# Performance work log

Measured on AMD Instinct MI355X. Metric: run time of the kernel, lower is better.

The kernel has to match this reference:

```python
import jax, jax.numpy as jnp
import numpy as np

N_E, E_DIM, BETA = 1024, 64, 0.25

def setup_inputs() -> dict:
    key = jax.random.key(0)
    k1, k2 = jax.random.split(key)
    z = jax.random.normal(k1, (16, 4096, E_DIM), dtype=jnp.float32)
    embedding = jax.random.uniform(k2, (N_E, E_DIM), dtype=jnp.float32,
                                   minval=-1.0 / 256, maxval=1.0 / 256)
    return {"z": z, "embedding": embedding}

def reference(z, embedding):
    # z: [B, S, D]; embedding: [n_e, D]
    zf = z.reshape(-1, E_DIM)  # [N, D]
    # squared euclidean distances: ||z||^2 + ||e||^2 - 2 z e^T -> [N, n_e]
    d = (jnp.sum(zf * zf, axis=1, keepdims=True)
         + jnp.sum(embedding * embedding, axis=1)
         - 2.0 * jnp.matmul(zf, embedding.T))
    min_encoding_indices = jnp.argmin(d, axis=1)  # [N]
    z_q = embedding[min_encoding_indices].reshape(z.shape)  # [B, S, D]
    sg = jax.lax.stop_gradient
    loss = (jnp.mean((z_q - sg(z)) ** 2)
            + BETA * jnp.mean((sg(z_q) - z) ** 2))
    z_q = z + sg(z_q - z)  # straight-through estimator
    return (loss, z_q, min_encoding_indices)
```

## Files before the change

### kernel.cpp

```cpp
#include <hip/hip_runtime.h>


#define D 64
#define NE 1024
#define SEGS 8
#define CPS 128
#define ROWS 64
#define TPB 512
#define LDS_STRIDE 68

__global__ __launch_bounds__(TPB, 6) void vq_kernel(const float* __restrict__ z,
                                                    const float* __restrict__ emb,
                                                    float* __restrict__ out_loss,
                                                    float* __restrict__ out_zq,
                                                    float* __restrict__ out_idx,
                                                    float loss_scale) {
    __shared__ float lds_z[ROWS * LDS_STRIDE];
    __shared__ float ee_lds[NE];
    __shared__ float smv[SEGS * ROWS];
    __shared__ int   smi[SEGS * ROWS];

    const int tid = threadIdx.x;
    const size_t blockRow = (size_t)blockIdx.x * ROWS;

    const float4* zg4 = (const float4*)(z + blockRow * D);
#pragma unroll
    for (int it = 0; it < 2; ++it) {
        int i = it * TPB + tid;
        int row = i >> 4, col = i & 15;
        float4 v = zg4[i];
        *(float4*)&lds_z[row * LDS_STRIDE + col * 4] = v;
    }

    {
#pragma clang fp contract(off)
#pragma unroll
        for (int cc = 0; cc < 2; ++cc) {
            const int j = tid + cc * TPB;
            const float4* e4 = (const float4*)(emb + ((size_t)j << 6));
            float4 a = e4[0], b = e4[1];
            float r[8];
            r[0] = a.x*a.x; r[1] = a.y*a.y; r[2] = a.z*a.z; r[3] = a.w*a.w;
            r[4] = b.x*b.x; r[5] = b.y*b.y; r[6] = b.z*b.z; r[7] = b.w*b.w;
#pragma unroll
            for (int g = 1; g < 8; ++g) {
                float4 c = e4[2*g], e = e4[2*g + 1];
                r[0] = r[0] + c.x*c.x; r[1] = r[1] + c.y*c.y;
                r[2] = r[2] + c.z*c.z; r[3] = r[3] + c.w*c.w;
                r[4] = r[4] + e.x*e.x; r[5] = r[5] + e.y*e.y;
                r[6] = r[6] + e.z*e.z; r[7] = r[7] + e.w*e.w;
            }
            ee_lds[j] = ((r[0]+r[1]) + (r[2]+r[3])) + ((r[4]+r[5]) + (r[6]+r[7]));
        }
    }
    __syncthreads();

    const int rrow = tid & (ROWS - 1);
    const int seg  = tid >> 6;

    float zr[D];
#pragma unroll
    for (int c = 0; c < 16; ++c) {
        float4 v = *(const float4*)&lds_z[rrow * LDS_STRIDE + c * 4];
        zr[4*c+0] = v.x; zr[4*c+1] = v.y; zr[4*c+2] = v.z; zr[4*c+3] = v.w;
    }

    float zz;
    {
#pragma clang fp contract(off)
        float r[8];
#pragma unroll
        for (int jj = 0; jj < 8; ++jj) { float t = zr[jj] * zr[jj]; r[jj] = t; }
#pragma unroll
        for (int i = 8; i < 64; i += 8) {
#pragma unroll
            for (int jj = 0; jj < 8; ++jj) { float t = zr[i+jj] * zr[i+jj]; r[jj] = r[jj] + t; }
        }
        zz = ((r[0]+r[1]) + (r[2]+r[3])) + ((r[4]+r[5]) + (r[6]+r[7]));
    }

    float minv = __builtin_inff();
    int mini = 0;
    const int jbase = __builtin_amdgcn_readfirstlane(seg * CPS);
#pragma unroll 2
    for (int jj = 0; jj < CPS; ++jj) {
        const int j = jbase + jj;
        const float4* ew4 = (const float4*)(emb + ((size_t)j << 6));
        float p0 = 0.f, p1 = 0.f, p2 = 0.f, p3 = 0.f;
#pragma unroll
        for (int c = 0; c < 16; ++c) {
            float4 e4 = ew4[c];
            p0 = fmaf(zr[4*c+0], e4.x, p0);
            p1 = fmaf(zr[4*c+1], e4.y, p1);
            p2 = fmaf(zr[4*c+2], e4.z, p2);
            p3 = fmaf(zr[4*c+3], e4.w, p3);
        }
        float dot = (p0 + p1) + (p2 + p3);
        float t1 = zz + ee_lds[j];
        float d = fmaf(-2.0f, dot, t1);
        if (d < minv) { minv = d; mini = j; }
    }

    smv[seg * ROWS + rrow] = minv;
    smi[seg * ROWS + rrow] = mini;
    __syncthreads();

    if (tid < ROWS) {
        float best = __builtin_inff();
        int bi = 0;
#pragma unroll
        for (int s = 0; s < SEGS; ++s) {
            float v = smv[s * ROWS + rrow];
            if (v < best) { best = v; bi = smi[s * ROWS + rrow]; }
        }

        const float4* qe4 = (const float4*)(emb + ((size_t)bi << 6));
        float s = 0.f;
#pragma unroll
        for (int c = 0; c < 16; ++c) {
            float4 q = qe4[c];
            float z0 = zr[4*c+0], z1 = zr[4*c+1], z2 = zr[4*c+2], z3 = zr[4*c+3];
            float d0 = q.x - z0, d1 = q.y - z1, d2 = q.z - z2, d3 = q.w - z3;
            s += d0*d0; s += d1*d1; s += d2*d2; s += d3*d3;
            float4 o;
            o.x = z0 + d0; o.y = z1 + d1; o.z = z2 + d2; o.w = z3 + d3;
            *(float4*)&lds_z[rrow * LDS_STRIDE + c * 4] = o;
        }
        out_idx[blockRow + rrow] = (float)bi;

#pragma unroll
        for (int off = 32; off; off >>= 1) s += __shfl_down(s, off);
        if (tid == 0) atomicAdd(out_loss, s * loss_scale);
    }
    __syncthreads();

    const size_t obase = blockRow * D;
#pragma unroll
    for (int it = 0; it < 8; ++it) {
        int i = it * TPB + tid;
        int row = i >> 6, col = i & 63;
        out_zq[obase + i] = lds_z[row * LDS_STRIDE + col];
    }
}

extern "C" void kernel_launch(void* const* d_in, const int* in_sizes, int n_in,
                              void* d_out, int out_size, void* d_ws, size_t ws_size,
                              hipStream_t stream) {
    const float* z   = (const float*)d_in[0];
    const float* emb = (const float*)d_in[1];
    const int nz = in_sizes[0];
    const int N  = nz / D;

    float* out      = (float*)d_out;
    float* out_zq   = out + 1;
    float* out_idx  = out + 1 + (size_t)nz;

    const float loss_scale = 1.25f / (float)nz;

    hipMemsetAsync(out, 0, sizeof(float), stream);
    vq_kernel<<<N / ROWS, TPB, 0, stream>>>(z, emb, out, out_zq, out_idx, loss_scale);
}
```

Baseline: 262.9 us.

## Stream codebook through LDS with double-buffered global_load_lds DMA

```diff
diff --git a/kernel.cpp b/kernel.cpp
--- a/kernel.cpp
+++ b/kernel.cpp
@@ -1,41 +1,52 @@
 #include <hip/hip_runtime.h>
+#include <stdint.h>
 
 
 #define D 64
 #define NE 1024
-#define SEGS 8
-#define CPS 128
+#define SEGS 4
+#define CPS 256
 #define ROWS 64
-#define TPB 512
-#define LDS_STRIDE 68
+#define TPB 256
+#define ZSTRIDE 68
 
-__global__ __launch_bounds__(TPB, 6) void vq_kernel(const float* __restrict__ z,
+#define WAIT_VMCNT1 0x0F71
+#define WAIT_VMCNT0 0x0F70
+#define WAIT_LGKM0  0xC07F
+
+typedef const __attribute__((address_space(1))) void* gas_t;
+typedef __attribute__((address_space(3))) void* las_t;
+
+__device__ __forceinline__ void dma_4rows(const float* gsrc, float* ldst, int lane) {
+    __builtin_amdgcn_global_load_lds((gas_t)(gsrc + lane * 4), (las_t)ldst, 16, 0, 0);
+}
+
+__global__ __launch_bounds__(TPB, 4) void vq_kernel(const float* __restrict__ z,
                                                     const float* __restrict__ emb,
                                                     float* __restrict__ out_loss,
                                                     float* __restrict__ out_zq,
                                                     float* __restrict__ out_idx,
                                                     float loss_scale) {
-    __shared__ float lds_z[ROWS * LDS_STRIDE];
-    __shared__ float ee_lds[NE];
-    __shared__ float smv[SEGS * ROWS];
-    __shared__ int   smi[SEGS * ROWS];
+    __shared__ __align__(16) float pool0[ROWS * ZSTRIDE];
+    __shared__ __align__(16) float pool1[NE];
 
-    const int tid = threadIdx.x;
+    const int tid  = threadIdx.x;
+    const int lane = tid & 63;
     const size_t blockRow = (size_t)blockIdx.x * ROWS;
 
     const float4* zg4 = (const float4*)(z + blockRow * D);
 #pragma unroll
-    for (int it = 0; it < 2; ++it) {
+    for (int it = 0; it < 4; ++it) {
         int i = it * TPB + tid;
         int row = i >> 4, col = i & 15;
         float4 v = zg4[i];
-        *(float4*)&lds_z[row * LDS_STRIDE + col * 4] = v;
+        *(float4*)&pool0[row * ZSTRIDE + col * 4] = v;
     }
 
     {
 #pragma clang fp contract(off)
 #pragma unroll
-        for (int cc = 0; cc < 2; ++cc) {
+        for (int cc = 0; cc < 4; ++cc) {
             const int j = tid + cc * TPB;
             const float4* e4 = (const float4*)(emb + ((size_t)j << 6));
             float4 a = e4[0], b = e4[1];
@@ -50,21 +61,17 @@
                 r[4] = r[4] + e.x*e.x; r[5] = r[5] + e.y*e.y;
                 r[6] = r[6] + e.z*e.z; r[7] = r[7] + e.w*e.w;
             }
-            ee_lds[j] = ((r[0]+r[1]) + (r[2]+r[3])) + ((r[4]+r[5]) + (r[6]+r[7]));
+            pool1[j] = ((r[0]+r[1]) + (r[2]+r[3])) + ((r[4]+r[5]) + (r[6]+r[7]));
         }
     }
     __syncthreads();
 
-    const int rrow = tid & (ROWS - 1);
-    const int seg  = tid >> 6;
-
     float zr[D];
 #pragma unroll
     for (int c = 0; c < 16; ++c) {
-        float4 v = *(const float4*)&lds_z[rrow * LDS_STRIDE + c * 4];
+        float4 v = *(const float4*)&pool0[lane * ZSTRIDE + c * 4];
         zr[4*c+0] = v.x; zr[4*c+1] = v.y; zr[4*c+2] = v.z; zr[4*c+3] = v.w;
     }
-
     float zz;
     {
 #pragma clang fp contract(off)
@@ -78,31 +85,51 @@
         }
         zz = ((r[0]+r[1]) + (r[2]+r[3])) + ((r[4]+r[5]) + (r[6]+r[7]));
     }
+    __syncthreads();
+
+    const int seg   = __builtin_amdgcn_readfirstlane(tid >> 6);
+    float* cbuf     = &pool0[seg * 512];
+    const int jbase = seg * CPS;
+    const float* gseg = emb + ((size_t)jbase << 6);
 
     float minv = __builtin_inff();
-    int mini = 0;
-    const int jbase = __builtin_amdgcn_readfirstlane(seg * CPS);
-#pragma unroll 2
-    for (int jj = 0; jj < CPS; ++jj) {
-        const int j = jbase + jj;
-        const float4* ew4 = (const float4*)(emb + ((size_t)j << 6));
-        float p0 = 0.f, p1 = 0.f, p2 = 0.f, p3 = 0.f;
+    int   mini = 0;
+
+    dma_4rows(gseg + 0 * 256, cbuf + 0,   lane);
+    dma_4rows(gseg + 1 * 256, cbuf + 256, lane);
+
+    for (int ch = 0; ch < 64; ++ch) {
+        if (ch == 63) __builtin_amdgcn_s_waitcnt(WAIT_VMCNT0);
+        else          __builtin_amdgcn_s_waitcnt(WAIT_VMCNT1);
+        __builtin_amdgcn_sched_barrier(0);
+        const float* cb = &cbuf[(ch & 1) * 256];
 #pragma unroll
-        for (int c = 0; c < 16; ++c) {
-            float4 e4 = ew4[c];
-            p0 = fmaf(zr[4*c+0], e4.x, p0);
-            p1 = fmaf(zr[4*c+1], e4.y, p1);
-            p2 = fmaf(zr[4*c+2], e4.z, p2);
-            p3 = fmaf(zr[4*c+3], e4.w, p3);
+        for (int cc = 0; cc < 4; ++cc) {
+            const int j = jbase + ch * 4 + cc;
+            float p0 = 0.f, p1 = 0.f, p2 = 0.f, p3 = 0.f;
+#pragma unroll
+            for (int c = 0; c < 16; ++c) {
+                float4 e4 = *(const float4*)&cb[cc * 64 + c * 4];
+                p0 = fmaf(zr[4*c+0], e4.x, p0);
+                p1 = fmaf(zr[4*c+1], e4.y, p1);
+                p2 = fmaf(zr[4*c+2], e4.z, p2);
+                p3 = fmaf(zr[4*c+3], e4.w, p3);
+            }
+            float dot = (p0 + p1) + (p2 + p3);
+            float t1 = zz + pool1[j];
+            float d = fmaf(-2.0f, dot, t1);
+            if (d < minv) { minv = d; mini = j; }
         }
-        float dot = (p0 + p1) + (p2 + p3);
-        float t1 = zz + ee_lds[j];
-        float d = fmaf(-2.0f, dot, t1);
-        if (d < minv) { minv = d; mini = j; }
+        if (ch < 62) {
+            __builtin_amdgcn_s_waitcnt(WAIT_LGKM0);
+            __builtin_amdgcn_sched_barrier(0);
+            dma_4rows(gseg + (ch + 2) * 256, cbuf + (ch & 1) * 256, lane);
+        }
     }
 
-    smv[seg * ROWS + rrow] = minv;
-    smi[seg * ROWS + rrow] = mini;
+    __syncthreads();
+    pool1[seg * 64 + lane]       = minv;
+    pool1[256 + seg * 64 + lane] = (float)mini;
     __syncthreads();
 
     if (tid < ROWS) {
@@ -110,8 +137,8 @@
         int bi = 0;
 #pragma unroll
         for (int s = 0; s < SEGS; ++s) {
-            float v = smv[s * ROWS + rrow];
-            if (v < best) { best = v; bi = smi[s * ROWS + rrow]; }
+            float v = pool1[s * 64 + tid];
+            if (v < best) { best = v; bi = (int)pool1[256 + s * 64 + tid]; }
         }
 
         const float4* qe4 = (const float4*)(emb + ((size_t)bi << 6));
@@ -124,9 +151,9 @@
             s += d0*d0; s += d1*d1; s += d2*d2; s += d3*d3;
             float4 o;
             o.x = z0 + d0; o.y = z1 + d1; o.z = z2 + d2; o.w = z3 + d3;
-            *(float4*)&lds_z[rrow * LDS_STRIDE + c * 4] = o;
+            *(float4*)&pool0[tid * ZSTRIDE + c * 4] = o;
         }
-        out_idx[blockRow + rrow] = (float)bi;
+        out_idx[blockRow + tid] = (float)bi;
 
 #pragma unroll
         for (int off = 32; off; off >>= 1) s += __shfl_down(s, off);
@@ -136,10 +163,10 @@
 
     const size_t obase = blockRow * D;
 #pragma unroll
-    for (int it = 0; it < 8; ++it) {
+    for (int it = 0; it < 16; ++it) {
         int i = it * TPB + tid;
         int row = i >> 6, col = i & 63;
-        out_zq[obase + i] = lds_z[row * LDS_STRIDE + col];
+        out_zq[obase + i] = pool0[row * ZSTRIDE + col];
     }
 }
 
```

After: 292.6 us. 11.3% more time.
